# Optimization experiments

Measured on AMD Instinct MI355X. Metric: run time of the kernel, lower is better.

The kernel has to match this reference:

```python
import jax, jax.numpy as jnp
import numpy as np

EPS = 1e-05  # module eps (both LayerNorm and mask-count denominator)


def setup_inputs() -> dict:
    key = jax.random.key(0)
    ks = jax.random.split(key, 6)
    b, m, n, dm, dh, dp = 1, 256, 384, 256, 32, 128
    x = jax.random.normal(ks[0], (b, m, n, dm), jnp.float32)
    mask = jnp.ones((b, m, n), dtype=bool)
    ln_g = jnp.ones((dm,), jnp.float32)
    ln_b = jnp.zeros((dm,), jnp.float32)
    wl = jax.random.normal(ks[1], (dm, dh), jnp.float32) * 0.02
    bl = jnp.zeros((dh,), jnp.float32)
    wr = jax.random.normal(ks[2], (dm, dh), jnp.float32) * 0.02
    br = jnp.zeros((dh,), jnp.float32)
    wo = jax.random.normal(ks[3], (dh * dh, dp), jnp.float32) * 0.02
    bo = jnp.zeros((dp,), jnp.float32)
    return dict(x=x, mask=mask, ln_g=ln_g, ln_b=ln_b, wl=wl, bl=bl,
                wr=wr, br=br, wo=wo, bo=bo)


def reference(x, mask, ln_g, ln_b, wl, bl, wr, br, wo, bo):
    # x: (b, m, i, dim_msa); mask: (b, m, i)
    mu = jnp.mean(x, axis=-1, keepdims=True)
    var = jnp.var(x, axis=-1, keepdims=True)
    xn = (x - mu) / jnp.sqrt(var + EPS) * ln_g + ln_b

    mf = mask.astype(x.dtype)  # (b, m, i)
    # mask_i * mask_j on the outer product == masking left and right separately
    left = (xn @ wl + bl) * mf[..., None]   # (b, m, i, dh)
    right = (xn @ wr + br) * mf[..., None]  # (b, m, j, dh)

    # sum over MSA depth m without materializing the (b,m,i,j,c,d) tensor
    outer = jnp.einsum('bmic,bmjd->bijcd', left, right)  # (b, i, j, dh, dh)
    b_, n_ = outer.shape[0], outer.shape[1]
    out = outer.reshape(b_, n_, n_, -1) @ wo + bo  # (b, i, j, dim_pairwise)

    # normalize by pairwise mask count (matches masked branch of the module)
    count = jnp.einsum('bmi,bmj->bij', mf, mf)[..., None]  # (b, i, j, 1)
    return out / (count + EPS)
```

## Files before the change

### kernel.cpp

```cpp
#include <hip/hip_runtime.h>
#include <hip/hip_bf16.h>

#define EPS 1e-5f
#define MM 256
#define NN 384
#define DM 256
#define DH 32
#define DP 128
#define NIC (NN*DH)

typedef __attribute__((ext_vector_type(8))) short short8;
typedef __attribute__((ext_vector_type(4))) float floatx4;

__device__ __forceinline__ void load16_to_lds(const void* gptr, void* lptr) {
    __builtin_amdgcn_global_load_lds(
        (const __attribute__((address_space(1))) void*)gptr,
        (__attribute__((address_space(3))) void*)lptr,
        16, 0, 0);
}

__device__ __forceinline__ unsigned short f2bf_bits(float f) {
    __hip_bfloat16 h = __float2bfloat16(f);
    union { __hip_bfloat16 h; unsigned short u; } cvt;
    cvt.h = h;
    return cvt.u;
}

__global__ __launch_bounds__(256) void k0a_woT(
    const float* __restrict__ wo, unsigned short* __restrict__ woT2)
{
    __shared__ float ts[64*129];
    const int s  = blockIdx.x >> 2;
    const int dg = blockIdx.x & 3;
    const int t  = threadIdx.x;
    #pragma unroll
    for (int g = 0; g < 32; g++) {
        int idx = g*256 + t;
        int row = idx >> 7, p = idx & 127;
        int ci = row >> 3, di = row & 7;
        int cd = (s*8 + ci)*32 + dg*8 + di;
        ts[row*129 + p] = wo[(size_t)cd*DP + p];
    }
    __syncthreads();
    int p = t >> 1, half = t & 1;
    #pragma unroll
    for (int dq = 0; dq < 4; dq++) {
        int di = half*4 + dq;
        #pragma unroll
        for (int cq = 0; cq < 2; cq++) {
            ushort4 u;
            u.x = f2bf_bits(ts[((cq*4+0)*8 + di)*129 + p]);
            u.y = f2bf_bits(ts[((cq*4+1)*8 + di)*129 + p]);
            u.z = f2bf_bits(ts[((cq*4+2)*8 + di)*129 + p]);
            u.w = f2bf_bits(ts[((cq*4+3)*8 + di)*129 + p]);
            *(ushort4*)&woT2[(size_t)p*1024 + s*256 + dg*64 + di*8 + cq*4] = u;
        }
    }
}

__global__ __launch_bounds__(256) void k0b_w(
    const float* __restrict__ wl, const float* __restrict__ bl,
    const float* __restrict__ wr, const float* __restrict__ br,
    unsigned short* __restrict__ WbT, float* __restrict__ bias)
{
    const int c = blockIdx.x, k = threadIdx.x;
    float v = (c < DH) ? wl[k*DH + c] : wr[k*DH + (c - DH)];
    WbT[c*256 + k] = f2bf_bits(v);
    if (c == 0 && k < 64) bias[k] = (k < DH) ? bl[k] : br[k - DH];
}

__global__ __launch_bounds__(384) void k2a_pack(
    const int* __restrict__ mask, unsigned int* __restrict__ pack)
{
    int tw = blockIdx.x, i = threadIdx.x;
    unsigned int wbits = 0;
    #pragma unroll
    for (int b = 0; b < 32; b++)
        wbits |= (mask[(tw*32 + b)*NN + i] != 0 ? 1u : 0u) << b;
    pack[i*8 + tw] = wbits;
}

__global__ __launch_bounds__(256) void k2_count(
    const unsigned int* __restrict__ pack, float* __restrict__ cinv)
{
    int id = blockIdx.x * 256 + threadIdx.x;
    int i = id / NN, j = id % NN;
    int s = 0;
    #pragma unroll
    for (int tw = 0; tw < 8; tw++)
        s += __popc(pack[i*8 + tw] & pack[j*8 + tw]);
    cinv[id] = 1.0f / ((float)s + EPS);
}

__global__ __launch_bounds__(256, 4) void k1_lnproj(
    const float* __restrict__ x, const int* __restrict__ mask,
    const float* __restrict__ ln_g, const float* __restrict__ ln_b,
    const unsigned short* __restrict__ WbTg, const float* __restrict__ bias,
    unsigned short* __restrict__ Lb, unsigned short* __restrict__ Rb)
{
    __shared__ unsigned short xns[64*264];
    __shared__ float mfs[64];

    const int i  = blockIdx.x;
    const int mc = blockIdx.y;
    const int t = threadIdx.x;
    const int l = t & 63, w = t >> 6;
    const int lc = l & 15, quad = l >> 4;
    const int sub = l >> 4, lc4 = l & 15;

    float4 gk[4], bk[4];
    #pragma unroll
    for (int g = 0; g < 4; g++) {
        gk[g] = *(const float4*)&ln_g[g*64 + lc4*4];
        bk[g] = *(const float4*)&ln_b[g*64 + lc4*4];
    }

    float4 v[4][4];
    #pragma unroll
    for (int rr = 0; rr < 4; rr++) {
        int mlocal = w*16 + rr*4 + sub;
        int m = mc*64 + mlocal;
        const float4* xr = (const float4*)&x[((size_t)m*NN + i)*DM];
        #pragma unroll
        for (int g = 0; g < 4; g++)
            v[rr][g] = xr[g*16 + lc4];
    }

    #pragma unroll
    for (int rr = 0; rr < 4; rr++) {
        int mlocal = w*16 + rr*4 + sub;
        int m = mc*64 + mlocal;
        float s = 0.f, s2 = 0.f;
        #pragma unroll
        for (int g = 0; g < 4; g++) {
            float4 vg = v[rr][g];
            s  += vg.x + vg.y + vg.z + vg.w;
            s2 += vg.x*vg.x + vg.y*vg.y + vg.z*vg.z + vg.w*vg.w;
        }
        #pragma unroll
        for (int off = 1; off < 16; off <<= 1) {
            s  += __shfl_xor(s,  off, 64);
            s2 += __shfl_xor(s2, off, 64);
        }
        float mu   = s * (1.0f/DM);
        float var  = s2 * (1.0f/DM) - mu*mu;
        float rstd = rsqrtf(var + EPS);
        #pragma unroll
        for (int g = 0; g < 4; g++) {
            float4 vg = v[rr][g];
            ushort4 u;
            u.x = f2bf_bits((vg.x - mu)*rstd*gk[g].x + bk[g].x);
            u.y = f2bf_bits((vg.y - mu)*rstd*gk[g].y + bk[g].y);
            u.z = f2bf_bits((vg.z - mu)*rstd*gk[g].z + bk[g].z);
            u.w = f2bf_bits((vg.w - mu)*rstd*gk[g].w + bk[g].w);
            *(ushort4*)&xns[mlocal*264 + g*64 + lc4*4] = u;
        }
        if (lc4 == 0) mfs[mlocal] = (mask[(size_t)m*NN + i] != 0) ? 1.0f : 0.0f;
    }
    __syncthreads();

    floatx4 acc[4];
    #pragma unroll
    for (int nt = 0; nt < 4; nt++) acc[nt] = (floatx4){0.f,0.f,0.f,0.f};
    #pragma unroll
    for (int ks = 0; ks < 8; ks++) {
        short8 af = *(const short8*)&xns[(w*16 + lc)*264 + ks*32 + quad*8];
        #pragma unroll
        for (int nt = 0; nt < 4; nt++) {
            short8 bf = *(const short8*)&WbTg[(nt*16 + lc)*256 + ks*32 + quad*8];
            acc[nt] = __builtin_amdgcn_mfma_f32_16x16x32_bf16(af, bf, acc[nt], 0, 0, 0);
        }
    }
    __syncthreads();

    unsigned short* tr = xns;
    #pragma unroll
    for (int nt = 0; nt < 4; nt++) {
        int c = nt*16 + lc;
        float bv = bias[c];
        #pragma unroll
        for (int rg = 0; rg < 4; rg++) {
            int mlocal = w*16 + quad*4 + rg;
            tr[c*72 + mlocal] = f2bf_bits((acc[nt][rg] + bv) * mfs[mlocal]);
        }
    }
    __syncthreads();

    {
        int c = t >> 2, seg = t & 3;
        unsigned short* dst = (c < DH)
            ? &Lb[((size_t)(i*DH + c))*MM + mc*64 + seg*16]
            : &Rb[((size_t)(i*DH + (c - DH)))*MM + mc*64 + seg*16];
        #pragma unroll
        for (int q = 0; q < 4; q++)
            *(ushort4*)&dst[q*4] = *(ushort4*)&tr[c*72 + seg*16 + q*4];
    }
}

__global__ __launch_bounds__(512, 2) void k3f_gemm(
    const unsigned short* __restrict__ Lb,
    const unsigned short* __restrict__ Rb,
    const unsigned short* __restrict__ woT2,
    const float* __restrict__ bo, const float* __restrict__ cinv,
    float* __restrict__ out)
{
    __shared__ short smem[32768];
    const int t = threadIdx.x;
    const int l = t & 63, w = t >> 6;
    const int wx = w & 3, wy = w >> 2;
    const int lc = l & 15, quad = l >> 4;

    int bid = blockIdx.x;
    int xcd = bid & 7;
    int local = bid >> 3;
    int bx = local / 6;
    int by = xcd * 6 + (local % 6);

    const size_t arow0 = (size_t)bx * 256;
    const size_t brow0 = (size_t)by * 256;

    const int pos0 = t, pos1 = 512 + t;
    const int line0 = pos0 >> 3, c0 = (pos0 & 7) ^ (line0 & 7);
    const int r0 = line0*2 + (c0 >> 2), k00 = (c0 & 3) * 8;
    const int line1 = pos1 >> 3, c1 = (pos1 & 7) ^ (line1 & 7);
    const int r1 = line1*2 + (c1 >> 2), k01 = (c1 & 3) * 8;

    const unsigned short* srcA0 = Lb + (arow0 + r0)*MM + k00;
    const unsigned short* srcA1 = Lb + (arow0 + r1)*MM + k01;
    const unsigned short* srcB0 = Rb + (brow0 + r0)*MM + k00;
    const unsigned short* srcB1 = Rb + (brow0 + r1)*MM + k01;

    floatx4 acc[8][4];
    #pragma unroll
    for (int a = 0; a < 8; a++)
        #pragma unroll
        for (int b = 0; b < 4; b++) acc[a][b] = (floatx4){0.f,0.f,0.f,0.f};

#define STAGE(bsel, step) do {                                           \
        char* sb = (char*)smem + (bsel)*32768;                           \
        load16_to_lds(srcA0 + (step)*32, sb + pos0*16);                  \
        load16_to_lds(srcA1 + (step)*32, sb + pos1*16);                  \
        load16_to_lds(srcB0 + (step)*32, sb + 16384 + pos0*16);          \
        load16_to_lds(srcB1 + (step)*32, sb + 16384 + pos1*16);          \
    } while (0)

    STAGE(0, 0);
    STAGE(1, 1);
    #pragma unroll
    for (int tstep = 0; tstep < 8; tstep++) {
        if (tstep < 7) asm volatile("s_waitcnt vmcnt(4)" ::: "memory");
        else           asm volatile("s_waitcnt vmcnt(0)" ::: "memory");
        __builtin_amdgcn_s_barrier();
        __builtin_amdgcn_sched_barrier(0);
        const char* Ab = (const char*)smem + (tstep & 1)*32768;
        const char* Bb = Ab + 16384;
        short8 bfr[4];
        #pragma unroll
        for (int nt = 0; nt < 4; nt++) {
            int r = wx*64 + nt*16 + lc;
            int li = r >> 1, cc = ((r & 1)*4 + quad) ^ (li & 7);
            bfr[nt] = *(const short8*)(Bb + li*128 + cc*16);
        }
        __builtin_amdgcn_s_setprio(1);
        #pragma unroll
        for (int mt = 0; mt < 8; mt++) {
            int r = wy*128 + mt*16 + lc;
            int li = r >> 1, cc = ((r & 1)*4 + quad) ^ (li & 7);
            short8 af = *(const short8*)(Ab + li*128 + cc*16);
            #pragma unroll
            for (int nt = 0; nt < 4; nt++)
                acc[mt][nt] = __builtin_amdgcn_mfma_f32_16x16x32_bf16(
                    af, bfr[nt], acc[mt][nt], 0, 0, 0);
        }
        __builtin_amdgcn_s_setprio(0);
        __builtin_amdgcn_s_barrier();
        __builtin_amdgcn_sched_barrier(0);
        if (tstep + 2 < 8) STAGE(tstep & 1, tstep + 2);
    }
#undef STAGE

    short* gp = smem;
    const int prow = w*16 + lc;
    floatx4 acc2[4];
    #pragma unroll
    for (int a = 0; a < 4; a++) acc2[a] = (floatx4){0.f,0.f,0.f,0.f};

    #pragma unroll
    for (int s = 0; s < 4; s++) {
        short8 b2r[8];
        #pragma unroll
        for (int ks = 0; ks < 8; ks++)
            b2r[ks] = *(const short8*)&woT2[(size_t)prow*1024 + s*256 + ks*32 + quad*8];

        if ((quad >> 1) == (s & 1)) {
            #pragma unroll
            for (int mmi = 0; mmi < 4; mmi++) {
                const int mt = (s >> 1) + mmi*2;
                #pragma unroll
                for (int nt = 0; nt < 4; nt++) {
                    int pair = (wy*4 + (mt >> 1))*8 + (wx*2 + (nt >> 1));
                    int d = (nt & 1)*16 + lc;
                    int kk = d*8 + (quad & 1)*4;
                    ushort4 u;
                    u.x = f2bf_bits(acc[mt][nt][0]);
                    u.y = f2bf_bits(acc[mt][nt][1]);
                    u.z = f2bf_bits(acc[mt][nt][2]);
                    u.w = f2bf_bits(acc[mt][nt][3]);
                    *(ushort4*)&gp[pair*264 + kk] = u;
                }
            }
        }
        __syncthreads();

        __builtin_amdgcn_s_setprio(1);
        #pragma unroll
        for (int ks = 0; ks < 8; ks++) {
            #pragma unroll
            for (int mt2 = 0; mt2 < 4; mt2++) {
                short8 a2 = *(const short8*)&gp[(mt2*16 + lc)*264 + ks*32 + quad*8];
                acc2[mt2] = __builtin_amdgcn_mfma_f32_16x16x32_bf16(
                    a2, b2r[ks], acc2[mt2], 0, 0, 0);
            }
        }
        __builtin_amdgcn_s_setprio(0);
        __syncthreads();
    }

    const float bv = bo[prow];
    #pragma unroll
    for (int mt2 = 0; mt2 < 4; mt2++) {
        #pragma unroll
        for (int rg = 0; rg < 4; rg++) {
            int pair = mt2*16 + quad*4 + rg;
            int i = bx*8 + (pair >> 3);
            int j = by*8 + (pair & 7);
            out[((size_t)(i*NN + j))*DP + prow] =
                (acc2[mt2][rg] + bv) * cinv[i*NN + j];
        }
    }
}

extern "C" void kernel_launch(void* const* d_in, const int* in_sizes, int n_in,
                              void* d_out, int out_size, void* d_ws, size_t ws_size,
                              hipStream_t stream)
{
    const float* x    = (const float*)d_in[0];
    const int*   mask = (const int*)d_in[1];
    const float* ln_g = (const float*)d_in[2];
    const float* ln_b = (const float*)d_in[3];
    const float* wl   = (const float*)d_in[4];
    const float* bl   = (const float*)d_in[5];
    const float* wr   = (const float*)d_in[6];
    const float* br   = (const float*)d_in[7];
    const float* wo   = (const float*)d_in[8];
    const float* bo   = (const float*)d_in[9];
    float* out = (float*)d_out;

    char* ws = (char*)d_ws;
    size_t off = 0;
    unsigned short* Lb   = (unsigned short*)(ws + off); off += (size_t)NIC*MM*2;
    unsigned short* Rb   = (unsigned short*)(ws + off); off += (size_t)NIC*MM*2;
    unsigned short* woT2 = (unsigned short*)(ws + off); off += (size_t)DP*1024*2;
    unsigned short* WbTg = (unsigned short*)(ws + off); off += (size_t)64*256*2;
    float*          bias = (float*)(ws + off);          off += 64*4;
    float*          cinv = (float*)(ws + off);          off += (size_t)NN*NN*4;
    unsigned int*   pack = (unsigned int*)Lb;

    k0a_woT<<<16, 256, 0, stream>>>(wo, woT2);
    k0b_w<<<64, 256, 0, stream>>>(wl, bl, wr, br, WbTg, bias);
    k2a_pack<<<8, 384, 0, stream>>>(mask, pack);
    k2_count<<<(NN*NN)/256, 256, 0, stream>>>(pack, cinv);
    k1_lnproj<<<dim3(NN, MM/64), 256, 0, stream>>>(x, mask, ln_g, ln_b, WbTg, bias, Lb, Rb);
    k3f_gemm<<<2304, 512, 0, stream>>>(Lb, Rb, woT2, bo, cinv, out);
}
```

Measured before the change: 356.2 us.

## Merge prep kernels into one launch and compute mask counts in GEMM epilogue

Combines the weight transpose, projection-weight conversion and mask bit-packing kernels into a single multi-role launch, removing three kernel launches. The separate pairwise count kernel and its cinv buffer are dropped; the final GEMM epilogue now computes the popcount of the packed mask words for each (i,j) pair and the reciprocal inline. The pack buffer moves to its own workspace slot instead of aliasing Lb. The launch_bounds occupancy hint on k1_lnproj is also removed. The epilogue does more loads and popcounts per output element in exchange for fewer launches and less global traffic.

```diff
diff --git a/kernel.cpp b/kernel.cpp
--- a/kernel.cpp
+++ b/kernel.cpp
@@ -26,73 +26,60 @@
     return cvt.u;
 }
 
-__global__ __launch_bounds__(256) void k0a_woT(
-    const float* __restrict__ wo, unsigned short* __restrict__ woT2)
+__global__ __launch_bounds__(256) void kprep(
+    const float* __restrict__ wo, unsigned short* __restrict__ woT2,
+    const float* __restrict__ wl, const float* __restrict__ bl,
+    const float* __restrict__ wr, const float* __restrict__ br,
+    unsigned short* __restrict__ WbT, float* __restrict__ bias,
+    const int* __restrict__ mask, unsigned int* __restrict__ pack)
 {
     __shared__ float ts[64*129];
-    const int s  = blockIdx.x >> 2;
-    const int dg = blockIdx.x & 3;
-    const int t  = threadIdx.x;
-    #pragma unroll
-    for (int g = 0; g < 32; g++) {
-        int idx = g*256 + t;
-        int row = idx >> 7, p = idx & 127;
-        int ci = row >> 3, di = row & 7;
-        int cd = (s*8 + ci)*32 + dg*8 + di;
-        ts[row*129 + p] = wo[(size_t)cd*DP + p];
-    }
-    __syncthreads();
-    int p = t >> 1, half = t & 1;
-    #pragma unroll
-    for (int dq = 0; dq < 4; dq++) {
-        int di = half*4 + dq;
-        #pragma unroll
-        for (int cq = 0; cq < 2; cq++) {
-            ushort4 u;
-            u.x = f2bf_bits(ts[((cq*4+0)*8 + di)*129 + p]);
-            u.y = f2bf_bits(ts[((cq*4+1)*8 + di)*129 + p]);
-            u.z = f2bf_bits(ts[((cq*4+2)*8 + di)*129 + p]);
-            u.w = f2bf_bits(ts[((cq*4+3)*8 + di)*129 + p]);
-            *(ushort4*)&woT2[(size_t)p*1024 + s*256 + dg*64 + di*8 + cq*4] = u;
-        }
-    }
-}
-
-__global__ __launch_bounds__(256) void k0b_w(
-    const float* __restrict__ wl, const float* __restrict__ bl,
-    const float* __restrict__ wr, const float* __restrict__ br,
-    unsigned short* __restrict__ WbT, float* __restrict__ bias)
-{
-    const int c = blockIdx.x, k = threadIdx.x;
-    float v = (c < DH) ? wl[k*DH + c] : wr[k*DH + (c - DH)];
-    WbT[c*256 + k] = f2bf_bits(v);
-    if (c == 0 && k < 64) bias[k] = (k < DH) ? bl[k] : br[k - DH];
-}
-
-__global__ __launch_bounds__(384) void k2a_pack(
-    const int* __restrict__ mask, unsigned int* __restrict__ pack)
-{
-    int tw = blockIdx.x, i = threadIdx.x;
-    unsigned int wbits = 0;
-    #pragma unroll
-    for (int b = 0; b < 32; b++)
-        wbits |= (mask[(tw*32 + b)*NN + i] != 0 ? 1u : 0u) << b;
-    pack[i*8 + tw] = wbits;
-}
-
-__global__ __launch_bounds__(256) void k2_count(
-    const unsigned int* __restrict__ pack, float* __restrict__ cinv)
-{
-    int id = blockIdx.x * 256 + threadIdx.x;
-    int i = id / NN, j = id % NN;
-    int s = 0;
-    #pragma unroll
-    for (int tw = 0; tw < 8; tw++)
-        s += __popc(pack[i*8 + tw] & pack[j*8 + tw]);
-    cinv[id] = 1.0f / ((float)s + EPS);
-}
-
-__global__ __launch_bounds__(256, 4) void k1_lnproj(
+    const int bid = blockIdx.x;
+    const int t   = threadIdx.x;
+
+    if (bid < 16) {
+        const int s  = bid >> 2;
+        const int dg = bid & 3;
+        #pragma unroll
+        for (int g = 0; g < 32; g++) {
+            int idx = g*256 + t;
+            int row = idx >> 7, p = idx & 127;
+            int ci = row >> 3, di = row & 7;
+            int cd = (s*8 + ci)*32 + dg*8 + di;
+            ts[row*129 + p] = wo[(size_t)cd*DP + p];
+        }
+        __syncthreads();
+        int p = t >> 1, half = t & 1;
+        #pragma unroll
+        for (int dq = 0; dq < 4; dq++) {
+            int di = half*4 + dq;
+            #pragma unroll
+            for (int cq = 0; cq < 2; cq++) {
+                ushort4 u;
+                u.x = f2bf_bits(ts[((cq*4+0)*8 + di)*129 + p]);
+                u.y = f2bf_bits(ts[((cq*4+1)*8 + di)*129 + p]);
+                u.z = f2bf_bits(ts[((cq*4+2)*8 + di)*129 + p]);
+                u.w = f2bf_bits(ts[((cq*4+3)*8 + di)*129 + p]);
+                *(ushort4*)&woT2[(size_t)p*1024 + s*256 + dg*64 + di*8 + cq*4] = u;
+            }
+        }
+    } else if (bid < 80) {
+        const int c = bid - 16, k = t;
+        float v = (c < DH) ? wl[k*DH + c] : wr[k*DH + (c - DH)];
+        WbT[c*256 + k] = f2bf_bits(v);
+        if (c == 0 && k < 64) bias[k] = (k < DH) ? bl[k] : br[k - DH];
+    } else {
+        int id = (bid - 80)*256 + t;
+        int i = id % NN, tw = id / NN;
+        unsigned int wbits = 0;
+        #pragma unroll
+        for (int b = 0; b < 32; b++)
+            wbits |= (mask[(tw*32 + b)*NN + i] != 0 ? 1u : 0u) << b;
+        pack[i*8 + tw] = wbits;
+    }
+}
+
+__global__ __launch_bounds__(256) void k1_lnproj(
     const float* __restrict__ x, const int* __restrict__ mask,
     const float* __restrict__ ln_g, const float* __restrict__ ln_b,
     const unsigned short* __restrict__ WbTg, const float* __restrict__ bias,
@@ -201,7 +188,7 @@
     const unsigned short* __restrict__ Lb,
     const unsigned short* __restrict__ Rb,
     const unsigned short* __restrict__ woT2,
-    const float* __restrict__ bo, const float* __restrict__ cinv,
+    const float* __restrict__ bo, const unsigned int* __restrict__ pack,
     float* __restrict__ out)
 {
     __shared__ short smem[32768];
@@ -334,8 +321,13 @@
             int pair = mt2*16 + quad*4 + rg;
             int i = bx*8 + (pair >> 3);
             int j = by*8 + (pair & 7);
+            int cnt = 0;
+            #pragma unroll
+            for (int tw = 0; tw < 8; tw++)
+                cnt += __popc(pack[i*8 + tw] & pack[j*8 + tw]);
+            float inv = 1.0f / ((float)cnt + EPS);
             out[((size_t)(i*NN + j))*DP + prow] =
-                (acc2[mt2][rg] + bv) * cinv[i*NN + j];
+                (acc2[mt2][rg] + bv) * inv;
         }
     }
 }
@@ -363,13 +355,9 @@
     unsigned short* woT2 = (unsigned short*)(ws + off); off += (size_t)DP*1024*2;
     unsigned short* WbTg = (unsigned short*)(ws + off); off += (size_t)64*256*2;
     float*          bias = (float*)(ws + off);          off += 64*4;
-    float*          cinv = (float*)(ws + off);          off += (size_t)NN*NN*4;
-    unsigned int*   pack = (unsigned int*)Lb;
-
-    k0a_woT<<<16, 256, 0, stream>>>(wo, woT2);
-    k0b_w<<<64, 256, 0, stream>>>(wl, bl, wr, br, WbTg, bias);
-    k2a_pack<<<8, 384, 0, stream>>>(mask, pack);
-    k2_count<<<(NN*NN)/256, 256, 0, stream>>>(pack, cinv);
+    unsigned int*   pack = (unsigned int*)(ws + off);   off += (size_t)NN*8*4;
+
+    kprep<<<92, 256, 0, stream>>>(wo, woT2, wl, bl, wr, br, WbTg, bias, mask, pack);
     k1_lnproj<<<dim3(NN, MM/64), 256, 0, stream>>>(x, mask, ln_g, ln_b, WbTg, bias, Lb, Rb);
-    k3f_gemm<<<2304, 512, 0, stream>>>(Lb, Rb, woT2, bo, cinv, out);
-}
+    k3f_gemm<<<2304, 512, 0, stream>>>(Lb, Rb, woT2, bo, pack, out);
+}
```

Result: slower. 382.1 us (+7.3%).
